# Kernel optimization log

Hardware: AMD Instinct MI355X
Metric: run time of the kernel (lower is better)

The kernel has to match this reference:

```python
import jax, jax.numpy as jnp
import numpy as np

D_MODEL = 256
K = 50                      # angle_k neighbors
TEMPERATURE = 10000.0
SCALE = 1.0
NUM_POS_FEATS = D_MODEL // 3 // 2 * 2   # 84
PADDING = D_MODEL - NUM_POS_FEATS * 3   # 4


def setup_inputs() -> dict:
    key = jax.random.key(0)
    ks = jax.random.split(key, 6)
    B, N, M = 4, 20000, 1024
    points = jax.random.normal(ks[0], (B, N, 3), jnp.float32)
    nodes = jax.random.normal(ks[1], (B, M, 3), jnp.float32)
    pn = jax.random.normal(ks[2], (B, N, 3), jnp.float32)
    nn_ = jax.random.normal(ks[3], (B, M, 3), jnp.float32)
    pn = pn / jnp.linalg.norm(pn, axis=-1, keepdims=True)
    nn_ = nn_ / jnp.linalg.norm(nn_, axis=-1, keepdims=True)
    W = jax.random.normal(ks[4], (4, D_MODEL), jnp.float32) * 0.5  # glo_proj weight (in,out)
    b = jax.random.normal(ks[5], (D_MODEL,), jnp.float32) * 0.1    # glo_proj bias
    return {"points": points, "nodes": nodes, "points_normals": pn,
            "nodes_normals": nn_, "W": W, "b": b}


def _signed_angle(v1, v2):
    sin_v = jnp.linalg.norm(jnp.cross(v1, v2), axis=-1)
    cos_v = jnp.sum(v1 * v2, axis=-1)
    ang = jnp.arctan2(sin_v, cos_v)
    return jnp.where(cos_v < 0, -ang, ang)


def _ppf_features(points, nodes, pn, nn_):
    # points (N,3), nodes (M,3); KNN gather then PPF angles -> (M,K,4)
    d2 = jnp.sum((nodes[:, None, :] - points[None, :, :]) ** 2, axis=-1)  # (M,N)
    _, knn_idx = jax.lax.top_k(-d2, K)          # (M,K) nearest points per node
    knn_pts = points[knn_idx]                   # (M,K,3) irregular gather
    knn_nrm = pn[knn_idx]                       # (M,K,3)
    ij = knn_pts - nodes[:, None, :]            # (M,K,3)
    d = jnp.linalg.norm(ij, axis=-1) * SCALE    # (M,K)
    n1 = jnp.broadcast_to(nn_[:, None, :], ij.shape)
    a_n1_d = _signed_angle(ij, n1)
    a_n2_d = _signed_angle(-ij, knn_nrm)
    a_n1_n2 = _signed_angle(n1, knn_nrm)
    return jnp.stack([d, a_n1_d, a_n2_d, a_n1_n2], axis=-1)  # (M,K,4)


def reference(points, nodes, points_normals, nodes_normals, W, b):
    # --- global embedding: PPF features -> Linear(4,D) -> max over K ---
    feats = jax.vmap(_ppf_features)(points, nodes, points_normals, nodes_normals)
    feats = jax.lax.stop_gradient(feats)        # original uses @torch.no_grad()
    glob = jnp.max(feats @ W + b, axis=-2)      # (B,M,D)
    # --- local embedding: sinusoidal position encoding of node coords ---
    dim_t = jnp.arange(NUM_POS_FEATS, dtype=jnp.float32)
    dim_t = TEMPERATURE ** (2.0 * jnp.floor(dim_t / 2.0) / NUM_POS_FEATS)
    pos = (nodes * SCALE)[..., None] / dim_t    # (B,M,3,F)
    pos_emb = jnp.stack([jnp.sin(pos[..., 0::2]), jnp.cos(pos[..., 1::2])], axis=-1)
    pos_emb = pos_emb.reshape(nodes.shape[0], nodes.shape[1], -1)  # (B,M,3*F)
    pos_emb = jnp.pad(pos_emb, [(0, 0), (0, 0), (0, PADDING)])     # (B,M,D)
    return glob, pos_emb
```

## Files before the change

### kernel.cpp

```cpp
#include <hip/hip_runtime.h>

#define N_PTS    20000
#define M_NODES  1024
#define BATCH    4
#define NNODE    (BATCH * M_NODES)
#define K_NN     50
#define D_MODEL  256
#define NPF      84
#define CAP      768
#define SELWIN   96
#define NSMP     2048
#define WLO      26
#define WHI      50
#define TN        32
#define KB_PPT    8
#define KB_CHUNK  2048
#define KB_NCHUNK 10
#define LOCAL_CAP 128
#define OVF_FLAG  (1 << 20)

__device__ __forceinline__ float signed_angle(float ax, float ay, float az,
                                              float bx, float by, float bz) {
    float cx = ay * bz - az * by;
    float cy = az * bx - ax * bz;
    float cz = ax * by - ay * bx;
    float s = sqrtf(cx * cx + cy * cy + cz * cz);
    float c = ax * bx + ay * by + az * bz;
    float a = atan2f(s, c);
    return (c < 0.0f) ? -a : a;
}

__global__ __launch_bounds__(256) void ka_thresh(
    const float* __restrict__ points, const float* __restrict__ nodes,
    float* __restrict__ tws, int* __restrict__ gcount, float* __restrict__ out)
{
    __shared__ float s3[NSMP * 3];
    const int tid  = threadIdx.x;
    const int w    = tid >> 6;
    const int lane = tid & 63;
    const int bm   = blockIdx.x * 4 + w;
    const int b    = bm >> 10;
    const float* pts = points + (size_t)b * N_PTS * 3;

    {
        const float4* src = (const float4*)pts;
        float4* dst = (float4*)s3;
        #pragma unroll
        for (int k = 0; k < 6; ++k)
            dst[tid + 256 * k] = src[tid + 256 * k];
    }
    __syncthreads();

    const float nx = nodes[(size_t)bm * 3 + 0];
    const float ny = nodes[(size_t)bm * 3 + 1];
    const float nz = nodes[(size_t)bm * 3 + 2];

    unsigned short keys[32];
    #pragma unroll
    for (int s = 0; s < 32; ++s) {
        int j = lane + 64 * s;
        float dx = s3[3 * j + 0] - nx;
        float dy = s3[3 * j + 1] - ny;
        float dz = s3[3 * j + 2] - nz;
        float d2 = dx * dx + dy * dy + dz * dz;
        keys[s] = (unsigned short)(__float_as_uint(d2) >> 16);
    }

    unsigned lo = 0, hi = 0x7F81u, v = 0;
    for (int it = 0; it < 16; ++it) {
        unsigned mid = lo + ((hi - lo) >> 1);
        int c = 0;
        #pragma unroll
        for (int s = 0; s < 32; ++s) c += (int)((unsigned)keys[s] < mid);
        for (int off = 32; off; off >>= 1) c += __shfl_down(c, off);
        c = __shfl(c, 0);
        if (c >= WLO && c <= WHI) { v = mid; break; }
        if (c < WLO) lo = mid; else hi = mid;
        if (hi - lo <= 1u) break;
    }
    if (v == 0) v = hi;
    if (lane == 0) { tws[bm] = __uint_as_float(v << 16); gcount[bm] = 0; }

    #pragma unroll
    for (int r = 0; r < 4; ++r) {
        int d = lane + 64 * r;
        float pv = 0.0f;
        if (d < 3 * NPF) {
            int c2 = d / NPF, rr = d - c2 * NPF, i = rr >> 1;
            float nc = (c2 == 0) ? nx : ((c2 == 1) ? ny : nz);
            const float L2_10000 = 13.287712379549449f;
            float tinv = exp2f(-L2_10000 * (float)i / 42.0f);
            float x = nc * tinv;
            pv = (rr & 1) ? cosf(x) : sinf(x);
        }
        out[(size_t)NNODE * D_MODEL + (size_t)bm * D_MODEL + d] = pv;
    }
}

__global__ __launch_bounds__(256) void kb_scan(
    const float* __restrict__ points, const float* __restrict__ nodes,
    const float* __restrict__ tws, int* __restrict__ gcount,
    unsigned short* __restrict__ cand)
{
    __shared__ unsigned short sbuf[TN][LOCAL_CAP];
    __shared__ int scnt[TN];
    __shared__ int sbase[TN];

    const int tile = blockIdx.x;
    const int ch   = blockIdx.y;
    const int ngb  = tile * TN;
    const int b    = ngb >> 10;
    const int tid  = threadIdx.x;
    const float* pts = points + (size_t)b * N_PTS * 3;

    if (tid < TN) scnt[tid] = 0;
    __syncthreads();

    const int j0 = ch * KB_CHUNK + tid * KB_PPT;
    float px[KB_PPT], py[KB_PPT], pz[KB_PPT], pp[KB_PPT];
    if (j0 < N_PTS) {
        const float4* s4 = (const float4*)(pts + (size_t)j0 * 3);
        float4 v0 = s4[0], v1 = s4[1], v2 = s4[2], v3 = s4[3], v4 = s4[4], v5 = s4[5];
        px[0]=v0.x; py[0]=v0.y; pz[0]=v0.z;
        px[1]=v0.w; py[1]=v1.x; pz[1]=v1.y;
        px[2]=v1.z; py[2]=v1.w; pz[2]=v2.x;
        px[3]=v2.y; py[3]=v2.z; pz[3]=v2.w;
        px[4]=v3.x; py[4]=v3.y; pz[4]=v3.z;
        px[5]=v3.w; py[5]=v4.x; pz[5]=v4.y;
        px[6]=v4.z; py[6]=v4.w; pz[6]=v5.x;
        px[7]=v5.y; py[7]=v5.z; pz[7]=v5.w;
    } else {
        #pragma unroll
        for (int p = 0; p < KB_PPT; ++p) { px[p]=1e18f; py[p]=1e18f; pz[p]=1e18f; }
    }
    #pragma unroll
    for (int p = 0; p < KB_PPT; ++p)
        pp[p] = px[p]*px[p] + py[p]*py[p] + pz[p]*pz[p];

    for (int n0 = 0; n0 < TN; n0 += 4) {
        float ax[4], ay[4], az[4], rhs[4];
        #pragma unroll
        for (int g = 0; g < 4; ++g) {
            int ng = ngb + n0 + g;
            float nx = nodes[ng * 3 + 0];
            float ny = nodes[ng * 3 + 1];
            float nz = nodes[ng * 3 + 2];
            float t  = tws[ng];
            ax[g] = -2.0f * nx; ay[g] = -2.0f * ny; az[g] = -2.0f * nz;
            rhs[g] = t * 1.0001f + 3e-5f - (nx*nx + ny*ny + nz*nz);
        }
        unsigned msk[4] = {0u, 0u, 0u, 0u};
        #pragma unroll
        for (int p = 0; p < KB_PPT; ++p) {
            #pragma unroll
            for (int g = 0; g < 4; ++g) {
                float s = fmaf(px[p], ax[g], fmaf(py[p], ay[g], fmaf(pz[p], az[g], pp[p])));
                msk[g] |= (s < rhs[g]) ? (1u << p) : 0u;
            }
        }
        #pragma unroll
        for (int g = 0; g < 4; ++g) {
            unsigned m = msk[g];
            if (m) {
                int n = n0 + g;
                do {
                    int p = __ffs(m) - 1; m &= m - 1;
                    int q = atomicAdd(&scnt[n], 1);
                    if (q < LOCAL_CAP) sbuf[n][q] = (unsigned short)(j0 + p);
                } while (m);
            }
        }
    }
    __syncthreads();

    if (tid < TN) {
        int c = scnt[tid];
        int flag = (c > LOCAL_CAP) ? OVF_FLAG : 0;
        sbase[tid] = atomicAdd(&gcount[ngb + tid], c + flag);
        scnt[tid] = (c < LOCAL_CAP) ? c : LOCAL_CAP;
    }
    __syncthreads();

    const int wv = tid >> 6, lane = tid & 63;
    #pragma unroll
    for (int nn = 0; nn < TN / 4; ++nn) {
        int n = wv * (TN / 4) + nn;
        int c = scnt[n], gb = sbase[n];
        for (int s = lane; s < c; s += 64) {
            int pos = gb + s;
            if (pos < CAP)
                cand[(size_t)(ngb + n) * CAP + pos] = sbuf[n][s];
        }
    }
}

__global__ __launch_bounds__(256) void kc_select(
    const float* __restrict__ points, const float* __restrict__ nodes,
    const float* __restrict__ pnrm, const float* __restrict__ nnrm,
    const float* __restrict__ W, const float* __restrict__ bias,
    const float* __restrict__ tws, const int* __restrict__ gcount,
    const unsigned short* __restrict__ cand, float* __restrict__ out)
{
    __shared__ unsigned long long skeys[4][CAP];
    __shared__ float4 f4v[4][K_NN];
    __shared__ unsigned short selidx[4][K_NN];

    const int tid  = threadIdx.x;
    const int wv   = tid >> 6;
    const int lane = tid & 63;
    const int bm   = blockIdx.x * 4 + wv;
    const int b    = bm >> 10;
    const float* pts = points + (size_t)b * N_PTS * 3;
    const float* pnr = pnrm   + (size_t)b * N_PTS * 3;
    const float nx  = nodes[(size_t)bm * 3 + 0];
    const float ny  = nodes[(size_t)bm * 3 + 1];
    const float nz  = nodes[(size_t)bm * 3 + 2];
    const float n1x = nnrm[(size_t)bm * 3 + 0];
    const float n1y = nnrm[(size_t)bm * 3 + 1];
    const float n1z = nnrm[(size_t)bm * 3 + 2];

    auto d2bits = [&](int i) -> unsigned int {
        float dx = pts[i * 3 + 0] - nx;
        float dy = pts[i * 3 + 1] - ny;
        float dz = pts[i * 3 + 2] - nz;
        return __float_as_uint(dx * dx + dy * dy + dz * dz);
    };

    if (lane < K_NN) selidx[wv][lane] = 0;

    const unsigned long long INVALID = ~0ull;
    int cnt = gcount[bm];
    int nsel = 0;

    if (cnt >= K_NN && cnt <= CAP) {
        const unsigned short* cp = cand + (size_t)bm * CAP;
        unsigned long long key[12];
        #pragma unroll
        for (int r = 0; r < 12; ++r) {
            int s = r * 64 + lane;
            key[r] = INVALID;
            if (s < cnt) {
                int i = (int)cp[s];
                key[r] = ((unsigned long long)d2bits(i) << 32) | (unsigned int)i;
            }
        }

        unsigned long long tcut = INVALID;
        bool conv = (cnt <= SELWIN);
        if (!conv) {
            unsigned lo = 0, hi = __float_as_uint(tws[bm]);
            for (int it = 0; it < 32 && !conv; ++it) {
                unsigned mid = lo + ((hi - lo) >> 1);
                unsigned long long tm = (unsigned long long)mid << 32;
                int c = 0;
                #pragma unroll
                for (int r = 0; r < 12; ++r)
                    c += (int)__popcll(__ballot(key[r] < tm));
                if (c >= K_NN && c <= SELWIN) { tcut = tm; conv = true; }
                else if (c < K_NN) lo = mid;
                else hi = mid;
                if (hi - lo <= 1u) break;
            }
        }

        int run = 0;
        #pragma unroll
        for (int r = 0; r < 12; ++r) {
            bool p = key[r] < tcut;
            unsigned long long mask = __ballot(p);
            if (p) {
                int q = run + (int)__popcll(mask & ((1ull << lane) - 1ull));
                skeys[wv][q] = key[r];
            }
            run += (int)__popcll(mask);
        }
        nsel = run;
    } else {
        unsigned tb = __float_as_uint(tws[bm]);
        unsigned lo = 0, hi = 0x7F000000u, good = 0;
        bool haveLo = false, haveHi = false;
        if (cnt < K_NN) { lo = tb; haveLo = true; }
        else            { hi = tb; haveHi = true; }
        unsigned cur = tb;
        for (int a = 0; a < 40 && !good; ++a) {
            if (haveLo && !haveHi) {
                cur = (cur < 0x7E800000u) ? cur + 0x00800000u : 0x7F000000u;
            } else if (haveHi && !haveLo) {
                cur = (cur >= 0x00800000u) ? cur - 0x00800000u : (cur >> 1);
            } else {
                cur = lo + ((hi - lo) >> 1);
                if (hi - lo <= 1u) { good = hi; break; }
            }
            float tf = __uint_as_float(cur);
            int c = 0;
            for (int i0 = lane; i0 < N_PTS; i0 += 64) {
                float dx = pts[i0 * 3 + 0] - nx;
                float dy = pts[i0 * 3 + 1] - ny;
                float dz = pts[i0 * 3 + 2] - nz;
                c += (int)(dx * dx + dy * dy + dz * dz < tf);
            }
            for (int off = 32; off; off >>= 1) c += __shfl_down(c, off);
            c = __shfl(c, 0);
            if (c >= K_NN && c <= CAP) good = cur;
            else if (c < K_NN) { lo = cur; haveLo = true; }
            else               { hi = cur; haveHi = true; }
        }
        if (!good) good = haveHi ? hi : 0x7F000000u;
        int run = 0;
        for (int base = 0; base < N_PTS; base += 64) {
            int i0 = base + lane;
            bool pred = false;
            unsigned kb2 = 0;
            if (i0 < N_PTS) { kb2 = d2bits(i0); pred = kb2 < good; }
            unsigned long long mask = __ballot(pred);
            if (pred) {
                int q = run + (int)__popcll(mask & ((1ull << lane) - 1ull));
                if (q < CAP)
                    skeys[wv][q] = ((unsigned long long)kb2 << 32) | (unsigned int)i0;
            }
            run += (int)__popcll(mask);
        }
        nsel = run < CAP ? run : CAP;
    }
    __syncthreads();

    for (int s = lane; s < nsel; s += 64) {
        unsigned long long mk = skeys[wv][s];
        int rank = 0;
        for (int j = 0; j < nsel; ++j) rank += (int)(skeys[wv][j] < mk);
        if (rank < K_NN) selidx[wv][rank] = (unsigned short)mk;
    }
    __syncthreads();

    if (lane < K_NN) {
        int i = (int)selidx[wv][lane];
        float pxx = pts[i * 3 + 0], pyy = pts[i * 3 + 1], pzz = pts[i * 3 + 2];
        float qx = pnr[i * 3 + 0], qy = pnr[i * 3 + 1], qz = pnr[i * 3 + 2];
        float ijx = pxx - nx, ijy = pyy - ny, ijz = pzz - nz;
        float d = sqrtf(ijx * ijx + ijy * ijy + ijz * ijz);
        f4v[wv][lane] = make_float4(d,
                                    signed_angle(ijx, ijy, ijz, n1x, n1y, n1z),
                                    signed_angle(-ijx, -ijy, -ijz, qx, qy, qz),
                                    signed_angle(n1x, n1y, n1z, qx, qy, qz));
    }
    __syncthreads();

    {
        float w0[4], w1[4], w2[4], w3[4], bb[4], mx[4];
        #pragma unroll
        for (int q = 0; q < 4; ++q) {
            int d = lane + 64 * q;
            w0[q] = W[d]; w1[q] = W[D_MODEL + d];
            w2[q] = W[2 * D_MODEL + d]; w3[q] = W[3 * D_MODEL + d];
            bb[q] = bias[d]; mx[q] = -INFINITY;
        }
        #pragma unroll 5
        for (int k = 0; k < K_NN; ++k) {
            float4 f = f4v[wv][k];
            #pragma unroll
            for (int q = 0; q < 4; ++q)
                mx[q] = fmaxf(mx[q], f.x * w0[q] + f.y * w1[q] + f.z * w2[q] + f.w * w3[q]);
        }
        #pragma unroll
        for (int q = 0; q < 4; ++q)
            out[(size_t)bm * D_MODEL + lane + 64 * q] = mx[q] + bb[q];
    }
}

extern "C" void kernel_launch(void* const* d_in, const int* in_sizes, int n_in,
                              void* d_out, int out_size, void* d_ws, size_t ws_size,
                              hipStream_t stream) {
    const float* points = (const float*)d_in[0];
    const float* nodes  = (const float*)d_in[1];
    const float* pn     = (const float*)d_in[2];
    const float* nn     = (const float*)d_in[3];
    const float* W      = (const float*)d_in[4];
    const float* bias   = (const float*)d_in[5];
    float* out = (float*)d_out;

    char* ws = (char*)d_ws;
    float* tws = (float*)ws;
    int* gcount = (int*)(ws + 16384);
    unsigned short* cand = (unsigned short*)(ws + 32768);

    ka_thresh<<<dim3(NNODE / 4), dim3(256), 0, stream>>>(points, nodes, tws, gcount, out);
    kb_scan<<<dim3(NNODE / TN, KB_NCHUNK), dim3(256), 0, stream>>>(points, nodes, tws, gcount, cand);
    kc_select<<<dim3(NNODE / 4), dim3(256), 0, stream>>>(points, nodes, pn, nn, W, bias,
                                                         tws, gcount, cand, out);
}
```

Before: 79.18 us.

## Replace shared-atomic candidate lists with per-node bitmasks and wave prefix-scan compaction

The scan kernel used to append every candidate point index to a per-node shared buffer through one shared-memory atomic per hit. It now records an 8-bit hit mask per thread and node, then each wave rebuilds the candidate indices with popcount, a shuffle prefix scan and a single global atomic per node. The threshold window constants (WLO/WHI, SELWIN) also shrink the target candidate count and widen the selection window, which should leave fewer candidates to write and sort. This removes contended shared atomics and the local overflow path, at the cost of scanning mask words for every node even when the node has few hits.

```diff
diff --git a/kernel.cpp b/kernel.cpp
--- a/kernel.cpp
+++ b/kernel.cpp
@@ -8,16 +8,14 @@
 #define D_MODEL  256
 #define NPF      84
 #define CAP      768
-#define SELWIN   96
+#define SELWIN   160
 #define NSMP     2048
-#define WLO      26
-#define WHI      50
+#define WLO      12
+#define WHI      24
 #define TN        32
 #define KB_PPT    8
 #define KB_CHUNK  2048
 #define KB_NCHUNK 10
-#define LOCAL_CAP 128
-#define OVF_FLAG  (1 << 20)
 
 __device__ __forceinline__ float signed_angle(float ax, float ay, float az,
                                               float bx, float by, float bz) {
@@ -102,9 +100,7 @@
     const float* __restrict__ tws, int* __restrict__ gcount,
     unsigned short* __restrict__ cand)
 {
-    __shared__ unsigned short sbuf[TN][LOCAL_CAP];
-    __shared__ int scnt[TN];
-    __shared__ int sbase[TN];
+    __shared__ unsigned char smask[TN][256];
 
     const int tile = blockIdx.x;
     const int ch   = blockIdx.y;
@@ -112,9 +108,6 @@
     const int b    = ngb >> 10;
     const int tid  = threadIdx.x;
     const float* pts = points + (size_t)b * N_PTS * 3;
-
-    if (tid < TN) scnt[tid] = 0;
-    __syncthreads();
 
     const int j0 = ch * KB_CHUNK + tid * KB_PPT;
     float px[KB_PPT], py[KB_PPT], pz[KB_PPT], pp[KB_PPT];
@@ -159,37 +152,37 @@
             }
         }
         #pragma unroll
-        for (int g = 0; g < 4; ++g) {
-            unsigned m = msk[g];
-            if (m) {
-                int n = n0 + g;
-                do {
-                    int p = __ffs(m) - 1; m &= m - 1;
-                    int q = atomicAdd(&scnt[n], 1);
-                    if (q < LOCAL_CAP) sbuf[n][q] = (unsigned short)(j0 + p);
-                } while (m);
-            }
-        }
-    }
-    __syncthreads();
-
-    if (tid < TN) {
-        int c = scnt[tid];
-        int flag = (c > LOCAL_CAP) ? OVF_FLAG : 0;
-        sbase[tid] = atomicAdd(&gcount[ngb + tid], c + flag);
-        scnt[tid] = (c < LOCAL_CAP) ? c : LOCAL_CAP;
+        for (int g = 0; g < 4; ++g)
+            smask[n0 + g][tid] = (unsigned char)msk[g];
     }
     __syncthreads();
 
     const int wv = tid >> 6, lane = tid & 63;
     #pragma unroll
-    for (int nn = 0; nn < TN / 4; ++nn) {
-        int n = wv * (TN / 4) + nn;
-        int c = scnt[n], gb = sbase[n];
-        for (int s = lane; s < c; s += 64) {
-            int pos = gb + s;
+    for (int nn2 = 0; nn2 < TN / 4; ++nn2) {
+        int n = wv * (TN / 4) + nn2;
+        unsigned long long wmask = 0;
+        if (lane < 32) wmask = ((const unsigned long long*)smask[n])[lane];
+        int c = (int)__popcll(wmask);
+        int inc = c;
+        #pragma unroll
+        for (int s = 1; s < 32; s <<= 1) {
+            int u = __shfl_up(inc, s);
+            if (lane >= s) inc += u;
+        }
+        int total = __shfl(inc, 31);
+        if (total == 0) continue;
+        int basep = 0;
+        if (lane == 0) basep = atomicAdd(&gcount[ngb + n], total);
+        basep = __shfl(basep, 0);
+        int pos = basep + inc - c;
+        while (wmask) {
+            int bit = (int)__builtin_ctzll(wmask);
+            wmask &= wmask - 1;
             if (pos < CAP)
-                cand[(size_t)(ngb + n) * CAP + pos] = sbuf[n][s];
+                cand[(size_t)(ngb + n) * CAP + pos] =
+                    (unsigned short)(ch * KB_CHUNK + lane * 64 + bit);
+            ++pos;
         }
     }
 }
```

Result: slower. 149.7 us (+89.1%).
